# Performance work log

Hardware: AMD Instinct MI355X
Metric: run time of the kernel (lower is better)

## Reference

```python
import jax, jax.numpy as jnp
import numpy as np

B = 16
CLS_OUT = 80
SCORE_THR = 0.05
IOU_THR = 0.65
MAX_NUM = 100
# FPN levels for a 1280x1280 input: (H, W, stride)
LEVELS = [(160, 160, 8), (80, 80, 16), (40, 40, 32)]
N = sum(h * w for h, w, _ in LEVELS)  # 33600


def make_priors():
    # mmdet MlvlPointGenerator(with_stride=True, offset=0): [x*stride, y*stride, stride, stride]
    ps = []
    for h, w, s in LEVELS:
        ys, xs = np.meshgrid(np.arange(h, dtype=np.float32), np.arange(w, dtype=np.float32), indexing='ij')
        st = np.full((h, w), float(s), dtype=np.float32)
        ps.append(np.stack([xs * s, ys * s, st, st], -1).reshape(-1, 4))
    return jnp.asarray(np.concatenate(ps, 0))


def setup_inputs() -> dict:
    key = jax.random.key(0)
    k1, k2, k3 = jax.random.split(key, 3)
    return {
        'cls_scores': jax.random.normal(k1, (B, N, CLS_OUT), dtype=jnp.float32),
        'bbox_preds': jax.random.normal(k2, (B, N, 4), dtype=jnp.float32),
        'objectness': jax.random.normal(k3, (B, N), dtype=jnp.float32),
        'priors': make_priors(),  # [N, 4]
    }


def _bbox_decode(priors, bbox_preds):
    # xy = pred_xy * stride + center;  wh = exp(pred_wh) * stride
    xys = bbox_preds[..., :2] * priors[:, 2:] + priors[:, :2]
    whs = jnp.exp(bbox_preds[..., 2:]) * priors[:, 2:]
    tl = xys - whs * 0.5
    br = xys + whs * 0.5
    return jnp.concatenate([tl, br], axis=-1)  # [B, N, 4] as (x1, y1, x2, y2)


def _iou_matrix(b1, b2):
    # b1: [M,4], b2: [M,4] -> [M,M], matching torch_cal_bbox_ious (no +1 offsets, eps=1e-8)
    x1 = jnp.maximum(b1[:, None, 0], b2[None, :, 0])
    y1 = jnp.maximum(b1[:, None, 1], b2[None, :, 1])
    x2 = jnp.minimum(b1[:, None, 2], b2[None, :, 2])
    y2 = jnp.minimum(b1[:, None, 3], b2[None, :, 3])
    inter = jnp.clip(x2 - x1, 0.0) * jnp.clip(y2 - y1, 0.0)
    a1 = (b1[:, 2] - b1[:, 0]) * (b1[:, 3] - b1[:, 1])
    a2 = (b2[:, 2] - b2[:, 0]) * (b2[:, 3] - b2[:, 1])
    union = a1[:, None] + a2[None, :] - inter
    return inter / (union + 1e-8)


def _nms_single(boxes, scores, labels, valid):
    # Take top MAX_NUM by score (invalid -> -inf), then class-aware greedy suppression.
    masked = jnp.where(valid, scores, -jnp.inf)
    order = jnp.argsort(-masked)[:MAX_NUM]
    b = boxes[order]          # [M,4]
    s = scores[order]         # [M]
    l = labels[order]         # [M]
    v = valid[order]          # [M]
    iou = _iou_matrix(b, b)
    same = l[:, None] == l[None, :]
    idx = jnp.arange(MAX_NUM)

    def body(i, keep):
        sup = keep[i] & same[i] & (iou[i] >= IOU_THR) & (idx > i)
        return keep & ~sup

    keep = jax.lax.fori_loop(0, MAX_NUM, body, v)
    dets = jnp.where(keep[:, None], jnp.concatenate([b, s[:, None]], -1), 0.0)  # [M,5]
    labs = jnp.where(keep, l, -1)
    return dets, labs, keep


def reference(cls_scores, bbox_preds, objectness, priors):
    cls = jax.nn.sigmoid(cls_scores)                  # [B,N,C]
    obj = jax.nn.sigmoid(objectness)                  # [B,N]
    bboxes = _bbox_decode(priors, bbox_preds)         # [B,N,4]
    max_scores = jnp.max(cls, axis=-1)                # [B,N]
    labels = jnp.argmax(cls, axis=-1).astype(jnp.int32)
    scores = max_scores * obj
    valid = scores >= SCORE_THR
    dets, labs, keep = jax.vmap(_nms_single)(bboxes, scores, labels, valid)
    out = jnp.concatenate([dets, labs[..., None].astype(jnp.float32)], -1)  # [B,MAX_NUM,6]
    return out, keep
```

## Files before the change

kernel.cpp:

```cpp
#include <hip/hip_runtime.h>
#include <cstddef>
#include <cstdint>

#define BB 16
#define NN 33600
#define CC 80
#define MAXN 100
#define NBINS 4096
#define MAXC 1024
#define SCORE_THR_F 0.05f
#define IOU_THR_F 0.65f

#define NCHUNK 525
#define K1_CPB 5
#define K1_GX (NCHUNK / K1_CPB)
#define K2T 1024
#define BPT (NBINS / K2T)
#define K2IT 9

typedef float f4 __attribute__((ext_vector_type(4)));

__global__ __launch_bounds__(256) void k1_score(const float* __restrict__ cls,
                                                const float* __restrict__ obj,
                                                float* __restrict__ masked,
                                                unsigned char* __restrict__ labels) {
  const int b = blockIdx.y;
  const int q = threadIdx.x & 3;
  const int r = threadIdx.x >> 2;
  const int c0 = blockIdx.x * K1_CPB;
#pragma unroll
  for (int cc = 0; cc < K1_CPB; cc++) {
    const int n = (c0 + cc) * 64 + r;
    const f4* row = (const f4*)(cls + ((size_t)b * NN + n) * CC);
    float m = -INFINITY;
    int lab = 0;
#pragma unroll
    for (int j = 0; j < 5; j++) {
      f4 v = __builtin_nontemporal_load(row + q + 4 * j);
      const int cb = (q + 4 * j) * 4;
      if (v.x > m) { m = v.x; lab = cb; }
      if (v.y > m) { m = v.y; lab = cb + 1; }
      if (v.z > m) { m = v.z; lab = cb + 2; }
      if (v.w > m) { m = v.w; lab = cb + 3; }
    }
#pragma unroll
    for (int d = 1; d < 4; d <<= 1) {
      float m2 = __shfl_xor(m, d, 4);
      int l2 = __shfl_xor(lab, d, 4);
      if (m2 > m || (m2 == m && l2 < lab)) { m = m2; lab = l2; }
    }
    if (q == 0) {
      const size_t bn = (size_t)b * NN + n;
      float o = obj[bn];
      float s = (1.0f / (1.0f + expf(-m))) * (1.0f / (1.0f + expf(-o)));
      masked[bn] = (s >= SCORE_THR_F) ? s : -INFINITY;
      labels[bn] = (unsigned char)lab;
    }
  }
}

__device__ __forceinline__ int score_bin(float s) {
  return min(NBINS - 1, (int)(s * (float)NBINS));
}

__global__ __launch_bounds__(K2T) void k2_all(const float* __restrict__ bbox,
                                              const float* __restrict__ priors,
                                              const float* __restrict__ masked,
                                              const unsigned char* __restrict__ labels,
                                              float* __restrict__ out) {
  const int b = blockIdx.x;
  const int tid = threadIdx.x;
  const int lane = tid & 63;
  const int wv = tid >> 6;

  __shared__ int hist[NBINS];
  __shared__ int wtot[K2T / 64];
  __shared__ int s_t, s_cnt;
  __shared__ float cs[MAXC];
  __shared__ int ci[MAXC];
  __shared__ int sel[MAXN];
  __shared__ float sb[MAXN][4];
  __shared__ float ssc[MAXN];
  __shared__ int slab[MAXN];
  __shared__ unsigned int sup[MAXN][4];
  __shared__ unsigned long long keep_lo, keep_hi;

  const f4* msc4 = (const f4*)(masked + (size_t)b * NN);

  f4 vals[K2IT];
#pragma unroll
  for (int it = 0; it < K2IT; it++) {
    const int i = tid + it * K2T;
    if (i < NN / 4) vals[it] = msc4[i];
  }

  for (int i = tid; i < NBINS; i += K2T) hist[i] = 0;
  for (int i = tid; i < MAXN * 4; i += K2T) ((unsigned int*)sup)[i] = 0;
  if (tid < MAXN) sel[tid] = -1;
  if (tid == 0) { s_t = 0; s_cnt = 0; }
  __syncthreads();

#pragma unroll
  for (int it = 0; it < K2IT; it++) {
    const int i = tid + it * K2T;
    if (i < NN / 4) {
      f4 v = vals[it];
      if (v.x >= SCORE_THR_F) atomicAdd(&hist[score_bin(v.x)], 1);
      if (v.y >= SCORE_THR_F) atomicAdd(&hist[score_bin(v.y)], 1);
      if (v.z >= SCORE_THR_F) atomicAdd(&hist[score_bin(v.z)], 1);
      if (v.w >= SCORE_THR_F) atomicAdd(&hist[score_bin(v.w)], 1);
    }
  }
  __syncthreads();

  int gsum = 0;
#pragma unroll
  for (int j = 0; j < BPT; j++) gsum += hist[tid * BPT + j];
  int sfx = gsum;
#pragma unroll
  for (int off = 1; off < 64; off <<= 1) {
    int t2 = __shfl_down(sfx, off);
    if (lane + off < 64) sfx += t2;
  }
  if (lane == 0) wtot[wv] = sfx;
  __syncthreads();
  int offw = 0;
#pragma unroll
  for (int w = 0; w < K2T / 64; w++) offw += (w > wv) ? wtot[w] : 0;
  const int S = sfx + offw;
  if (S >= MAXN && S - gsum < MAXN) {
    int running = S - gsum;
    for (int bin = tid * BPT + BPT - 1; bin >= tid * BPT; bin--) {
      running += hist[bin];
      if (running >= MAXN) { s_t = bin; break; }
    }
  }
  __syncthreads();
  const int t = s_t;

#pragma unroll
  for (int it = 0; it < K2IT; it++) {
    const int i = tid + it * K2T;
    if (i < NN / 4) {
      f4 v = vals[it];
      const int base = i * 4;
      if (v.x >= SCORE_THR_F && score_bin(v.x) >= t) {
        int p = atomicAdd(&s_cnt, 1); if (p < MAXC) { cs[p] = v.x; ci[p] = base; }
      }
      if (v.y >= SCORE_THR_F && score_bin(v.y) >= t) {
        int p = atomicAdd(&s_cnt, 1); if (p < MAXC) { cs[p] = v.y; ci[p] = base + 1; }
      }
      if (v.z >= SCORE_THR_F && score_bin(v.z) >= t) {
        int p = atomicAdd(&s_cnt, 1); if (p < MAXC) { cs[p] = v.z; ci[p] = base + 2; }
      }
      if (v.w >= SCORE_THR_F && score_bin(v.w) >= t) {
        int p = atomicAdd(&s_cnt, 1); if (p < MAXC) { cs[p] = v.w; ci[p] = base + 3; }
      }
    }
  }
  __syncthreads();
  const int C = min(s_cnt, MAXC);

  for (int i = tid; i < C; i += K2T) {
    float si = cs[i]; int ii = ci[i];
    int r = 0;
    for (int j = 0; j < C; j++) {
      float sj = cs[j]; int ij = ci[j];
      r += (sj > si) || (sj == si && ij < ii);
    }
    if (r < MAXN) { sel[r] = ii; ssc[r] = si; }
  }
  __syncthreads();

  if (tid < MAXN) {
    int idx = sel[tid];
    if (idx >= 0) {
      f4 p = ((const f4*)priors)[idx];
      f4 d = ((const f4*)bbox)[(size_t)b * NN + idx];
      float cx = d.x * p.z + p.x;
      float cy = d.y * p.w + p.y;
      float hw = expf(d.z) * p.z * 0.5f;
      float hh = expf(d.w) * p.w * 0.5f;
      sb[tid][0] = cx - hw; sb[tid][1] = cy - hh;
      sb[tid][2] = cx + hw; sb[tid][3] = cy + hh;
      slab[tid] = labels[(size_t)b * NN + idx];
    } else {
      sb[tid][0] = 0.f; sb[tid][1] = 0.f; sb[tid][2] = 0.f; sb[tid][3] = 0.f;
      ssc[tid] = 0.f; slab[tid] = -1;
    }
  }
  __syncthreads();

  for (int p = tid; p < MAXN * MAXN; p += K2T) {
    int i = p / MAXN, j = p % MAXN;
    if (j > i && sel[i] >= 0 && sel[j] >= 0 && slab[i] == slab[j]) {
      float xx1 = fmaxf(sb[i][0], sb[j][0]);
      float yy1 = fmaxf(sb[i][1], sb[j][1]);
      float xx2 = fminf(sb[i][2], sb[j][2]);
      float yy2 = fminf(sb[i][3], sb[j][3]);
      float inter = fmaxf(xx2 - xx1, 0.f) * fmaxf(yy2 - yy1, 0.f);
      float ai = (sb[i][2] - sb[i][0]) * (sb[i][3] - sb[i][1]);
      float aj = (sb[j][2] - sb[j][0]) * (sb[j][3] - sb[j][1]);
      float iou = inter / (ai + aj - inter + 1e-8f);
      if (iou >= IOU_THR_F) atomicOr(&sup[i][j >> 5], 1u << (j & 31));
    }
  }
  __syncthreads();

  if (tid < 64) {
    unsigned a0 = sup[lane][0], a1 = sup[lane][1], a2 = sup[lane][2], a3 = sup[lane][3];
    unsigned b0 = 0, b1 = 0, b2 = 0, b3 = 0;
    if (lane + 64 < MAXN) {
      b0 = sup[lane + 64][0]; b1 = sup[lane + 64][1];
      b2 = sup[lane + 64][2]; b3 = sup[lane + 64][3];
    }
    unsigned long long lo = __ballot(sel[lane] >= 0);
    unsigned long long hi = __ballot(lane + 64 < MAXN && sel[lane + 64] >= 0);
    for (int i = 0; i < MAXN; i++) {
      bool kb = (i < 64) ? ((lo >> i) & 1ull) : ((hi >> (i - 64)) & 1ull);
      if (kb) {
        unsigned s0, s1, s2, s3;
        if (i < 64) {
          s0 = (unsigned)__shfl((int)a0, i); s1 = (unsigned)__shfl((int)a1, i);
          s2 = (unsigned)__shfl((int)a2, i); s3 = (unsigned)__shfl((int)a3, i);
        } else {
          s0 = (unsigned)__shfl((int)b0, i - 64); s1 = (unsigned)__shfl((int)b1, i - 64);
          s2 = (unsigned)__shfl((int)b2, i - 64); s3 = (unsigned)__shfl((int)b3, i - 64);
        }
        lo &= ~(((unsigned long long)s1 << 32) | s0);
        hi &= ~(((unsigned long long)s3 << 32) | s2);
      }
    }
    if (lane == 0) { keep_lo = lo; keep_hi = hi; }
  }
  __syncthreads();

  if (tid < MAXN) {
    int k = tid;
    unsigned long long kw = (k < 64) ? keep_lo : keep_hi;
    int kbit = (k < 64) ? k : k - 64;
    bool kp = (kw >> kbit) & 1ull;
    float* row = out + ((size_t)b * MAXN + k) * 6;
    if (kp) {
      row[0] = sb[k][0]; row[1] = sb[k][1]; row[2] = sb[k][2]; row[3] = sb[k][3];
      row[4] = ssc[k];   row[5] = (float)slab[k];
    } else {
      row[0] = 0.f; row[1] = 0.f; row[2] = 0.f; row[3] = 0.f;
      row[4] = 0.f; row[5] = -1.f;
    }
    out[(size_t)BB * MAXN * 6 + (size_t)b * MAXN + k] = kp ? 1.0f : 0.0f;
  }
}

extern "C" void kernel_launch(void* const* d_in, const int* in_sizes, int n_in,
                              void* d_out, int out_size, void* d_ws, size_t ws_size,
                              hipStream_t stream) {
  const float* cls    = (const float*)d_in[0];
  const float* bbox   = (const float*)d_in[1];
  const float* obj    = (const float*)d_in[2];
  const float* priors = (const float*)d_in[3];
  float* out = (float*)d_out;
  float* masked = (float*)d_ws;
  unsigned char* labels = (unsigned char*)(masked + (size_t)BB * NN);

  k1_score<<<dim3(K1_GX, BB), 256, 0, stream>>>(cls, obj, masked, labels);
  k2_all<<<BB, K2T, 0, stream>>>(bbox, priors, masked, labels, out);
}
```

Baseline: 264.5 us.

## Fuse score and NMS kernels with last-block-per-batch completion counter

Merges the scoring kernel and the per-image top-k/NMS kernel into one launch. Each block scores its chunk, then bumps a per-batch atomic counter, and the last block to finish runs the histogram, selection and NMS for that image. This removes the second kernel launch and lets tail work overlap with other images still being scored. In exchange the selection stage runs with 256 threads instead of 1024, the histogram is halved to 2048 bins, and a memset is added to reset the counters.

After: 601.4 us. 127% more time.

```diff
diff --git a/kernel.cpp b/kernel.cpp
--- a/kernel.cpp
+++ b/kernel.cpp
@@ -6,7 +6,7 @@
 #define NN 33600
 #define CC 80
 #define MAXN 100
-#define NBINS 4096
+#define NBINS 2048
 #define MAXC 1024
 #define SCORE_THR_F 0.05f
 #define IOU_THR_F 0.65f
@@ -14,102 +14,100 @@
 #define NCHUNK 525
 #define K1_CPB 5
 #define K1_GX (NCHUNK / K1_CPB)
-#define K2T 1024
-#define BPT (NBINS / K2T)
-#define K2IT 9
+#define KT 256
+#define BPT (NBINS / KT)
 
 typedef float f4 __attribute__((ext_vector_type(4)));
-
-__global__ __launch_bounds__(256) void k1_score(const float* __restrict__ cls,
-                                                const float* __restrict__ obj,
-                                                float* __restrict__ masked,
-                                                unsigned char* __restrict__ labels) {
-  const int b = blockIdx.y;
-  const int q = threadIdx.x & 3;
-  const int r = threadIdx.x >> 2;
-  const int c0 = blockIdx.x * K1_CPB;
-#pragma unroll
-  for (int cc = 0; cc < K1_CPB; cc++) {
-    const int n = (c0 + cc) * 64 + r;
-    const f4* row = (const f4*)(cls + ((size_t)b * NN + n) * CC);
-    float m = -INFINITY;
-    int lab = 0;
-#pragma unroll
-    for (int j = 0; j < 5; j++) {
-      f4 v = __builtin_nontemporal_load(row + q + 4 * j);
-      const int cb = (q + 4 * j) * 4;
-      if (v.x > m) { m = v.x; lab = cb; }
-      if (v.y > m) { m = v.y; lab = cb + 1; }
-      if (v.z > m) { m = v.z; lab = cb + 2; }
-      if (v.w > m) { m = v.w; lab = cb + 3; }
-    }
-#pragma unroll
-    for (int d = 1; d < 4; d <<= 1) {
-      float m2 = __shfl_xor(m, d, 4);
-      int l2 = __shfl_xor(lab, d, 4);
-      if (m2 > m || (m2 == m && l2 < lab)) { m = m2; lab = l2; }
-    }
-    if (q == 0) {
-      const size_t bn = (size_t)b * NN + n;
-      float o = obj[bn];
-      float s = (1.0f / (1.0f + expf(-m))) * (1.0f / (1.0f + expf(-o)));
-      masked[bn] = (s >= SCORE_THR_F) ? s : -INFINITY;
-      labels[bn] = (unsigned char)lab;
-    }
-  }
-}
 
 __device__ __forceinline__ int score_bin(float s) {
   return min(NBINS - 1, (int)(s * (float)NBINS));
 }
 
-__global__ __launch_bounds__(K2T) void k2_all(const float* __restrict__ bbox,
-                                              const float* __restrict__ priors,
-                                              const float* __restrict__ masked,
-                                              const unsigned char* __restrict__ labels,
-                                              float* __restrict__ out) {
-  const int b = blockIdx.x;
+__global__ __launch_bounds__(KT, 4) void k_fused(const float* __restrict__ cls,
+                                                 const float* __restrict__ bbox,
+                                                 const float* __restrict__ obj,
+                                                 const float* __restrict__ priors,
+                                                 float* __restrict__ masked,
+                                                 unsigned char* __restrict__ labels,
+                                                 unsigned int* __restrict__ done,
+                                                 float* __restrict__ out) {
+  const int b = blockIdx.y;
   const int tid = threadIdx.x;
-  const int lane = tid & 63;
-  const int wv = tid >> 6;
 
   __shared__ int hist[NBINS];
-  __shared__ int wtot[K2T / 64];
-  __shared__ int s_t, s_cnt;
+  __shared__ int wtot[KT / 64];
+  __shared__ int s_t, s_cnt, s_last;
   __shared__ float cs[MAXC];
   __shared__ int ci[MAXC];
   __shared__ int sel[MAXN];
-  __shared__ float sb[MAXN][4];
+  __shared__ f4 sbox[MAXN];
   __shared__ float ssc[MAXN];
   __shared__ int slab[MAXN];
   __shared__ unsigned int sup[MAXN][4];
   __shared__ unsigned long long keep_lo, keep_hi;
 
+  {
+    const int q = tid & 3;
+    const int r = tid >> 2;
+    const int c0 = blockIdx.x * K1_CPB;
+#pragma unroll
+    for (int cc = 0; cc < K1_CPB; cc++) {
+      const int n = (c0 + cc) * 64 + r;
+      const f4* row = (const f4*)(cls + ((size_t)b * NN + n) * CC);
+      float m = -INFINITY;
+      int lab = 0;
+#pragma unroll
+      for (int j = 0; j < 5; j++) {
+        f4 v = __builtin_nontemporal_load(row + q + 4 * j);
+        const int cb = (q + 4 * j) * 4;
+        if (v.x > m) { m = v.x; lab = cb; }
+        if (v.y > m) { m = v.y; lab = cb + 1; }
+        if (v.z > m) { m = v.z; lab = cb + 2; }
+        if (v.w > m) { m = v.w; lab = cb + 3; }
+      }
+#pragma unroll
+      for (int d = 1; d < 4; d <<= 1) {
+        float m2 = __shfl_xor(m, d, 4);
+        int l2 = __shfl_xor(lab, d, 4);
+        if (m2 > m || (m2 == m && l2 < lab)) { m = m2; lab = l2; }
+      }
+      if (q == 0) {
+        const size_t bn = (size_t)b * NN + n;
+        float o = obj[bn];
+        float s = (1.0f / (1.0f + expf(-m))) * (1.0f / (1.0f + expf(-o)));
+        masked[bn] = (s >= SCORE_THR_F) ? s : -INFINITY;
+        labels[bn] = (unsigned char)lab;
+      }
+    }
+  }
+
+  __threadfence();
+  __syncthreads();
+  if (tid == 0) {
+    unsigned int old = atomicAdd(&done[b], 1u);
+    s_last = (old == (unsigned)(K1_GX - 1)) ? 1 : 0;
+  }
+  __syncthreads();
+  if (!s_last) return;
+  __threadfence();
+
+  const int lane = tid & 63;
+  const int wv = tid >> 6;
   const f4* msc4 = (const f4*)(masked + (size_t)b * NN);
 
-  f4 vals[K2IT];
-#pragma unroll
-  for (int it = 0; it < K2IT; it++) {
-    const int i = tid + it * K2T;
-    if (i < NN / 4) vals[it] = msc4[i];
-  }
-
-  for (int i = tid; i < NBINS; i += K2T) hist[i] = 0;
-  for (int i = tid; i < MAXN * 4; i += K2T) ((unsigned int*)sup)[i] = 0;
+  for (int i = tid; i < NBINS; i += KT) hist[i] = 0;
+  for (int i = tid; i < MAXN * 4; i += KT) ((unsigned int*)sup)[i] = 0;
   if (tid < MAXN) sel[tid] = -1;
   if (tid == 0) { s_t = 0; s_cnt = 0; }
   __syncthreads();
 
-#pragma unroll
-  for (int it = 0; it < K2IT; it++) {
-    const int i = tid + it * K2T;
-    if (i < NN / 4) {
-      f4 v = vals[it];
-      if (v.x >= SCORE_THR_F) atomicAdd(&hist[score_bin(v.x)], 1);
-      if (v.y >= SCORE_THR_F) atomicAdd(&hist[score_bin(v.y)], 1);
-      if (v.z >= SCORE_THR_F) atomicAdd(&hist[score_bin(v.z)], 1);
-      if (v.w >= SCORE_THR_F) atomicAdd(&hist[score_bin(v.w)], 1);
-    }
+#pragma unroll 4
+  for (int i = tid; i < NN / 4; i += KT) {
+    f4 v = msc4[i];
+    if (v.x >= SCORE_THR_F) atomicAdd(&hist[score_bin(v.x)], 1);
+    if (v.y >= SCORE_THR_F) atomicAdd(&hist[score_bin(v.y)], 1);
+    if (v.z >= SCORE_THR_F) atomicAdd(&hist[score_bin(v.z)], 1);
+    if (v.w >= SCORE_THR_F) atomicAdd(&hist[score_bin(v.w)], 1);
   }
   __syncthreads();
 
@@ -126,7 +124,7 @@
   __syncthreads();
   int offw = 0;
 #pragma unroll
-  for (int w = 0; w < K2T / 64; w++) offw += (w > wv) ? wtot[w] : 0;
+  for (int w = 0; w < KT / 64; w++) offw += (w > wv) ? wtot[w] : 0;
   const int S = sfx + offw;
   if (S >= MAXN && S - gsum < MAXN) {
     int running = S - gsum;
@@ -138,30 +136,27 @@
   __syncthreads();
   const int t = s_t;
 
-#pragma unroll
-  for (int it = 0; it < K2IT; it++) {
-    const int i = tid + it * K2T;
-    if (i < NN / 4) {
-      f4 v = vals[it];
-      const int base = i * 4;
-      if (v.x >= SCORE_THR_F && score_bin(v.x) >= t) {
-        int p = atomicAdd(&s_cnt, 1); if (p < MAXC) { cs[p] = v.x; ci[p] = base; }
-      }
-      if (v.y >= SCORE_THR_F && score_bin(v.y) >= t) {
-        int p = atomicAdd(&s_cnt, 1); if (p < MAXC) { cs[p] = v.y; ci[p] = base + 1; }
-      }
-      if (v.z >= SCORE_THR_F && score_bin(v.z) >= t) {
-        int p = atomicAdd(&s_cnt, 1); if (p < MAXC) { cs[p] = v.z; ci[p] = base + 2; }
-      }
-      if (v.w >= SCORE_THR_F && score_bin(v.w) >= t) {
-        int p = atomicAdd(&s_cnt, 1); if (p < MAXC) { cs[p] = v.w; ci[p] = base + 3; }
-      }
+#pragma unroll 4
+  for (int i = tid; i < NN / 4; i += KT) {
+    f4 v = msc4[i];
+    const int base = i * 4;
+    if (v.x >= SCORE_THR_F && score_bin(v.x) >= t) {
+      int p = atomicAdd(&s_cnt, 1); if (p < MAXC) { cs[p] = v.x; ci[p] = base; }
+    }
+    if (v.y >= SCORE_THR_F && score_bin(v.y) >= t) {
+      int p = atomicAdd(&s_cnt, 1); if (p < MAXC) { cs[p] = v.y; ci[p] = base + 1; }
+    }
+    if (v.z >= SCORE_THR_F && score_bin(v.z) >= t) {
+      int p = atomicAdd(&s_cnt, 1); if (p < MAXC) { cs[p] = v.z; ci[p] = base + 2; }
+    }
+    if (v.w >= SCORE_THR_F && score_bin(v.w) >= t) {
+      int p = atomicAdd(&s_cnt, 1); if (p < MAXC) { cs[p] = v.w; ci[p] = base + 3; }
     }
   }
   __syncthreads();
   const int C = min(s_cnt, MAXC);
 
-  for (int i = tid; i < C; i += K2T) {
+  for (int i = tid; i < C; i += KT) {
     float si = cs[i]; int ii = ci[i];
     int r = 0;
     for (int j = 0; j < C; j++) {
@@ -181,26 +176,27 @@
       float cy = d.y * p.w + p.y;
       float hw = expf(d.z) * p.z * 0.5f;
       float hh = expf(d.w) * p.w * 0.5f;
-      sb[tid][0] = cx - hw; sb[tid][1] = cy - hh;
-      sb[tid][2] = cx + hw; sb[tid][3] = cy + hh;
+      f4 bx; bx.x = cx - hw; bx.y = cy - hh; bx.z = cx + hw; bx.w = cy + hh;
+      sbox[tid] = bx;
       slab[tid] = labels[(size_t)b * NN + idx];
     } else {
-      sb[tid][0] = 0.f; sb[tid][1] = 0.f; sb[tid][2] = 0.f; sb[tid][3] = 0.f;
-      ssc[tid] = 0.f; slab[tid] = -1;
-    }
-  }
-  __syncthreads();
-
-  for (int p = tid; p < MAXN * MAXN; p += K2T) {
+      f4 z; z.x = 0.f; z.y = 0.f; z.z = 0.f; z.w = 0.f;
+      sbox[tid] = z; ssc[tid] = 0.f; slab[tid] = -1;
+    }
+  }
+  __syncthreads();
+
+  for (int p = tid; p < MAXN * MAXN; p += KT) {
     int i = p / MAXN, j = p % MAXN;
     if (j > i && sel[i] >= 0 && sel[j] >= 0 && slab[i] == slab[j]) {
-      float xx1 = fmaxf(sb[i][0], sb[j][0]);
-      float yy1 = fmaxf(sb[i][1], sb[j][1]);
-      float xx2 = fminf(sb[i][2], sb[j][2]);
-      float yy2 = fminf(sb[i][3], sb[j][3]);
+      f4 bi = sbox[i], bj = sbox[j];
+      float xx1 = fmaxf(bi.x, bj.x);
+      float yy1 = fmaxf(bi.y, bj.y);
+      float xx2 = fminf(bi.z, bj.z);
+      float yy2 = fminf(bi.w, bj.w);
       float inter = fmaxf(xx2 - xx1, 0.f) * fmaxf(yy2 - yy1, 0.f);
-      float ai = (sb[i][2] - sb[i][0]) * (sb[i][3] - sb[i][1]);
-      float aj = (sb[j][2] - sb[j][0]) * (sb[j][3] - sb[j][1]);
+      float ai = (bi.z - bi.x) * (bi.w - bi.y);
+      float aj = (bj.z - bj.x) * (bj.w - bj.y);
       float iou = inter / (ai + aj - inter + 1e-8f);
       if (iou >= IOU_THR_F) atomicOr(&sup[i][j >> 5], 1u << (j & 31));
     }
@@ -241,9 +237,10 @@
     int kbit = (k < 64) ? k : k - 64;
     bool kp = (kw >> kbit) & 1ull;
     float* row = out + ((size_t)b * MAXN + k) * 6;
+    f4 bx = sbox[k];
     if (kp) {
-      row[0] = sb[k][0]; row[1] = sb[k][1]; row[2] = sb[k][2]; row[3] = sb[k][3];
-      row[4] = ssc[k];   row[5] = (float)slab[k];
+      row[0] = bx.x; row[1] = bx.y; row[2] = bx.z; row[3] = bx.w;
+      row[4] = ssc[k]; row[5] = (float)slab[k];
     } else {
       row[0] = 0.f; row[1] = 0.f; row[2] = 0.f; row[3] = 0.f;
       row[4] = 0.f; row[5] = -1.f;
@@ -262,7 +259,9 @@
   float* out = (float*)d_out;
   float* masked = (float*)d_ws;
   unsigned char* labels = (unsigned char*)(masked + (size_t)BB * NN);
-
-  k1_score<<<dim3(K1_GX, BB), 256, 0, stream>>>(cls, obj, masked, labels);
-  k2_all<<<BB, K2T, 0, stream>>>(bbox, priors, masked, labels, out);
+  unsigned int* done = (unsigned int*)(labels + (size_t)BB * NN);
+
+  hipMemsetAsync(done, 0, BB * sizeof(unsigned int), stream);
+  k_fused<<<dim3(K1_GX, BB), KT, 0, stream>>>(cls, bbox, obj, priors,
+                                              masked, labels, done, out);
 }
```
